# Performance work log

Hardware: AMD Instinct MI355X
Metric: run time of the kernel (lower is better)

## Reference

```python
import jax, jax.numpy as jnp
import numpy as np

D_MODEL = 1024
B, N = 2, 4096
EPS = 1e-4


def setup_inputs() -> dict:
    key = jax.random.key(0)
    ks = jax.random.split(key, 8)
    s = 1.0 / np.sqrt(D_MODEL)
    return {
        "x": jax.random.normal(ks[0], (B, N, D_MODEL), dtype=jnp.float32),
        "Wq": jax.random.normal(ks[1], (D_MODEL, D_MODEL), dtype=jnp.float32) * s,
        "bq": jax.random.normal(ks[2], (D_MODEL,), dtype=jnp.float32) * 0.01,
        "Wk": jax.random.normal(ks[3], (D_MODEL, D_MODEL), dtype=jnp.float32) * s,
        "bk": jax.random.normal(ks[4], (D_MODEL,), dtype=jnp.float32) * 0.01,
        "Wv": jax.random.normal(ks[5], (D_MODEL, D_MODEL), dtype=jnp.float32) * s,
        "bv": jax.random.normal(ks[6], (D_MODEL,), dtype=jnp.float32) * 0.01,
        "alpha": jnp.float32(1.5),
        "lam": jnp.float32(12.0),
    }


def reference(x, Wq, bq, Wk, bk, Wv, bv, alpha, lam):
    # CSOCKernelAttention.forward
    Bb, n, d = x.shape
    # torch nn.Linear: y = x @ W.T + b
    q = jnp.einsum("bnd,ed->bne", x, Wq) + bq
    k = jnp.einsum("bnd,ed->bne", x, Wk) + bk
    v = jnp.einsum("bnd,ed->bne", x, Wv) + bv
    idx = jnp.arange(n, dtype=jnp.float32)
    r = jnp.abs(idx[:, None] - idx[None, :])  # [N, N]
    # K(r) = (r + eps)^(-|alpha|) * exp(-r / |lambda|)
    K = (r + EPS) ** (-jnp.abs(alpha)) * jnp.exp(-r / jnp.abs(lam))  # [N, N]
    logits = jnp.einsum("bqd,bkd->bqk", q, k) / jnp.sqrt(jnp.float32(d))
    logits = logits * K[None]
    attn = jax.nn.softmax(logits, axis=-1)
    out = jnp.einsum("bqk,bkd->bqd", attn, v)
    return (out, attn, K)
```

## Files before the change

### kernel.cpp

```cpp
#include <hip/hip_runtime.h>
#include <hip/hip_bf16.h>
#include <cstdint>
#include <cstddef>

#define D_MODEL 1024
#define SEQ_N   4096
#define BATCH   2
#define BAND    256
#define NELEM   ((size_t)BATCH * SEQ_N * D_MODEL)

typedef __attribute__((ext_vector_type(4))) float  floatx4;
typedef __attribute__((ext_vector_type(8))) short  short8;
typedef __attribute__((ext_vector_type(4))) short  short4v;

__device__ __forceinline__ unsigned short f2bf(float f) {
  unsigned u = __float_as_uint(f);
  u += 0x7FFFu + ((u >> 16) & 1u);
  return (unsigned short)(u >> 16);
}
__device__ __forceinline__ float bf2f(unsigned short u) {
  return __uint_as_float(((unsigned)u) << 16);
}

__global__ __launch_bounds__(256)
void fused_prep(const float* __restrict__ x,
                const float* __restrict__ Wq, const float* __restrict__ Wk,
                const float* __restrict__ Wv, const float* __restrict__ bv,
                const float* __restrict__ alpha_p, const float* __restrict__ lam_p,
                unsigned short* __restrict__ xb,
                unsigned short* __restrict__ Bcat2,
                unsigned short* __restrict__ wqT,
                unsigned short* __restrict__ wkT,
                float* __restrict__ bias2,
                float* __restrict__ K1d)
{
  __shared__ unsigned short Tld[64][66];
  int bid = blockIdx.x, tid = threadIdx.x;
  if (bid < 4096) {
    int i = bid * 256 + tid;
    const floatx4* s4 = (const floatx4*)x;
    floatx4 a = s4[i * 2], b = s4[i * 2 + 1];
    short8 pk;
    pk[0] = (short)f2bf(a[0]); pk[1] = (short)f2bf(a[1]);
    pk[2] = (short)f2bf(a[2]); pk[3] = (short)f2bf(a[3]);
    pk[4] = (short)f2bf(b[0]); pk[5] = (short)f2bf(b[1]);
    pk[6] = (short)f2bf(b[2]); pk[7] = (short)f2bf(b[3]);
    *(short8*)(xb + (size_t)i * 8) = pk;
  } else if (bid < 4608) {
    int i = (bid - 4096) * 256 + tid;
    const floatx4* s4 = (const floatx4*)Wv;
    floatx4 a = s4[i * 2], b = s4[i * 2 + 1];
    short8 pk;
    pk[0] = (short)f2bf(a[0]); pk[1] = (short)f2bf(a[1]);
    pk[2] = (short)f2bf(a[2]); pk[3] = (short)f2bf(a[3]);
    pk[4] = (short)f2bf(b[0]); pk[5] = (short)f2bf(b[1]);
    pk[6] = (short)f2bf(b[2]); pk[7] = (short)f2bf(b[3]);
    *(short8*)(Bcat2 + (size_t)D_MODEL * D_MODEL + (size_t)i * 8) = pk;
  } else if (bid < 5120) {
    int u = bid - 4608;
    const float* src = (u < 256) ? Wq : Wk;
    unsigned short* dst = (u < 256) ? wqT : wkT;
    int t = u & 255;
    int tr = t >> 4, tc = t & 15;
    int rl = tid >> 2, cc = (tid & 3) * 16;
    const float* sp = src + (size_t)(tr * 64 + rl) * D_MODEL + tc * 64 + cc;
#pragma unroll
    for (int q4 = 0; q4 < 4; ++q4) {
      floatx4 v = *(const floatx4*)(sp + q4 * 4);
#pragma unroll
      for (int e = 0; e < 4; ++e) Tld[cc + q4 * 4 + e][rl] = f2bf(v[e]);
    }
    __syncthreads();
    int cl = tid >> 2, rchunk = (tid & 3) * 16;
    short8 o0, o1;
#pragma unroll
    for (int e = 0; e < 8; ++e) { o0[e] = (short)Tld[cl][rchunk + e]; o1[e] = (short)Tld[cl][rchunk + 8 + e]; }
    unsigned short* dp = dst + (size_t)(tc * 64 + cl) * D_MODEL + tr * 64 + rchunk;
    *(short8*)dp = o0;
    *(short8*)(dp + 8) = o1;
  } else {
    int t = (bid - 5120) * 256 + tid;
    if (t < SEQ_N) {
      float a   = fabsf(alpha_p[0]);
      float lam = fabsf(lam_p[0]);
      float rf  = (float)t;
      K1d[t] = powf(rf + 1e-4f, -a) * expf(-rf / lam);
    }
    int v = t - SEQ_N;
    if (v >= 0 && v < D_MODEL) bias2[D_MODEL + v] = bv[v];
  }
}

__global__ __launch_bounds__(256)
void wg_kernel(const unsigned short* __restrict__ wkT,
               const unsigned short* __restrict__ wqT,
               const float* __restrict__ bq, const float* __restrict__ bk,
               unsigned short* __restrict__ Mt,
               float* __restrict__ bias2, float* __restrict__ wqv)
{
  __shared__ unsigned short As[64 * 32];
  __shared__ unsigned short Bs[64 * 32];
  const int bid = blockIdx.x, tid = threadIdx.x;
  const int lane = tid & 63, wave = tid >> 6;

  if (bid < 512) {
    const int idx = bid * 4 + wave;
    const int d = idx & (D_MODEL - 1);
    const bool isK = idx < D_MODEL;
    const unsigned short* row = (isK ? wkT : wqT) + (size_t)d * D_MODEL + lane * 16;
    const float* b = isK ? bq : bk;
    float s = 0.f;
    short8 v0 = *(const short8*)row, v1 = *(const short8*)(row + 8);
#pragma unroll
    for (int e = 0; e < 8; ++e) {
      s += bf2f((unsigned short)v0[e]) * b[lane * 16 + e];
      s += bf2f((unsigned short)v1[e]) * b[lane * 16 + 8 + e];
    }
#pragma unroll
    for (int o = 32; o; o >>= 1) s += __shfl_xor(s, o);
    if (lane == 0) { if (isK) bias2[d] = s; else wqv[d] = s; }
    return;
  }

  int flat = bid - 512;
  int w = (flat & 7) * 32 + (flat >> 3);
  int bx = w % 16, by = w / 16;
  const int bm0 = by * 64, bn0 = bx * 64;
  const int wm = (wave >> 1) * 32, wn = (wave & 1) * 32;

  floatx4 acc[2][2] = {};
  for (int k0 = 0; k0 < D_MODEL; k0 += 32) {
    {
      int bu = wave * 64;
      int u  = bu + lane;
      const unsigned short* srcA = wkT + (size_t)(bm0 + (u >> 2)) * D_MODEL + k0 + (u & 3) * 8;
      __builtin_amdgcn_global_load_lds((const __attribute__((address_space(1))) void*)srcA,
                                       (__attribute__((address_space(3))) void*)(As + bu * 8), 16, 0, 0);
      const unsigned short* srcB = wqT + (size_t)(bn0 + (u >> 2)) * D_MODEL + k0 + (u & 3) * 8;
      __builtin_amdgcn_global_load_lds((const __attribute__((address_space(1))) void*)srcB,
                                       (__attribute__((address_space(3))) void*)(Bs + bu * 8), 16, 0, 0);
    }
    __syncthreads();
    short8 af[2], bf[2];
#pragma unroll
    for (int i = 0; i < 2; ++i)
      af[i] = *(const short8*)(As + (wm + i * 16 + (lane & 15)) * 32 + (lane >> 4) * 8);
#pragma unroll
    for (int j = 0; j < 2; ++j)
      bf[j] = *(const short8*)(Bs + (wn + j * 16 + (lane & 15)) * 32 + (lane >> 4) * 8);
#pragma unroll
    for (int i = 0; i < 2; ++i)
#pragma unroll
      for (int j = 0; j < 2; ++j)
        acc[i][j] = __builtin_amdgcn_mfma_f32_16x16x32_bf16(af[i], bf[j], acc[i][j], 0, 0, 0);
    __syncthreads();
  }
#pragma unroll
  for (int i = 0; i < 2; ++i) {
#pragma unroll
    for (int j = 0; j < 2; ++j) {
      int col   = bn0 + wn + j * 16 + (lane & 15);
      int rbase = bm0 + wm + i * 16 + (lane >> 4) * 4;
#pragma unroll
      for (int r = 0; r < 4; ++r)
        Mt[(size_t)(rbase + r) * D_MODEL + col] = f2bf(acc[i][j][r]);
    }
  }
}

__global__ __launch_bounds__(256)
void rc_kernel(const unsigned short* __restrict__ vT,
               const unsigned short* __restrict__ xb,
               const float* __restrict__ wqv,
               const float* __restrict__ bq, const float* __restrict__ bk,
               float* __restrict__ colsumV, float* __restrict__ rho)
{
  const int bid = blockIdx.x;
  const int lane = threadIdx.x & 63, wave = threadIdx.x >> 6;
  if (bid < 512) {
    const int idx = bid * 4 + wave;
    const int d = idx >> 1, b = idx & 1;
    const unsigned short* p = vT + (size_t)d * (BATCH * SEQ_N) + b * SEQ_N;
    float s = 0.f;
#pragma unroll
    for (int it = 0; it < 8; ++it) {
      short8 v = *(const short8*)(p + (size_t)(it * 512 + lane * 8));
#pragma unroll
      for (int e = 0; e < 8; ++e) s += bf2f((unsigned short)v[e]);
    }
#pragma unroll
    for (int o = 32; o; o >>= 1) s += __shfl_xor(s, o);
    if (lane == 0) colsumV[b * D_MODEL + d] = s;
    return;
  }
  const int gi = (bid - 512) * 4 + wave;
  const unsigned short* xr = xb + (size_t)gi * D_MODEL + lane * 16;
  float s1 = 0.f, s2 = 0.f;
  short8 v0 = *(const short8*)xr, v1 = *(const short8*)(xr + 8);
#pragma unroll
  for (int e = 0; e < 8; ++e) {
    s1 += bf2f((unsigned short)v0[e]) * wqv[lane * 16 + e];
    s1 += bf2f((unsigned short)v1[e]) * wqv[lane * 16 + 8 + e];
  }
#pragma unroll
  for (int e = 0; e < 16; ++e)
    s2 += bq[lane * 16 + e] * bk[lane * 16 + e];
  float s = s1 + s2;
#pragma unroll
  for (int o = 32; o; o >>= 1) s += __shfl_xor(s, o);
  if (lane == 0) rho[gi] = s;
}

__global__ void k1d_kernel(float* __restrict__ K1d,
                           const float* __restrict__ alpha_p,
                           const float* __restrict__ lam_p) {
  int r = blockIdx.x * blockDim.x + threadIdx.x;
  if (r >= SEQ_N) return;
  float a   = fabsf(alpha_p[0]);
  float lam = fabsf(lam_p[0]);
  float rf  = (float)r;
  K1d[r] = powf(rf + 1e-4f, -a) * expf(-rf / lam);
}

__global__ __launch_bounds__(256) void writeK_kernel(float* __restrict__ Kout,
                                                     const float* __restrict__ K1d) {
  size_t t = (size_t)blockIdx.x * 256 + threadIdx.x;
  size_t f = t * 4;
  int i = (int)(f >> 12);
  int j = (int)(f & 4095);
  floatx4 v;
#pragma unroll
  for (int e = 0; e < 4; ++e) {
    int d = i - (j + e); d = d < 0 ? -d : d;
    v[e] = K1d[d];
  }
  __builtin_nontemporal_store(v, (floatx4*)(Kout + f));
}

__global__ __launch_bounds__(256)
void uv_gemm(const unsigned short* __restrict__ xb,
             const unsigned short* __restrict__ Bcat2,
             const float* __restrict__ bias2,
             unsigned short* __restrict__ ub,
             unsigned short* __restrict__ vT)
{
  __shared__ unsigned short As[128 * 64];
  __shared__ unsigned short Bs[128 * 64];
  const int tid = threadIdx.x, lane = tid & 63, wave = tid >> 6;

  int gx = (int)gridDim.x, gy = (int)gridDim.y;
  int total = gx * gy;
  int flat  = (int)blockIdx.y * gx + (int)blockIdx.x;
  int w     = (flat & 7) * (total >> 3) + (flat >> 3);
  int bx = w % gx, by = w / gx;
  const int bm0 = by * 128;
  const int bn0 = bx * 128;
  const int wm = (wave >> 1) * 64, wn = (wave & 1) * 64;
  const bool isU = (bn0 < D_MODEL);

  floatx4 acc[4][4] = {};
  for (int k0 = 0; k0 < D_MODEL; k0 += 64) {
#pragma unroll
    for (int t = 0; t < 4; ++t) {
      int bu  = wave * 64 + t * 256;
      int u   = bu + lane;
      int row = u >> 3;
      int c   = (u & 7) ^ (row & 7);
      const unsigned short* srcA = xb + (size_t)(bm0 + row) * D_MODEL + k0 + c * 8;
      __builtin_amdgcn_global_load_lds((const __attribute__((address_space(1))) void*)srcA,
                                       (__attribute__((address_space(3))) void*)(As + bu * 8), 16, 0, 0);
      const unsigned short* srcB = Bcat2 + (size_t)(bn0 + row) * D_MODEL + k0 + c * 8;
      __builtin_amdgcn_global_load_lds((const __attribute__((address_space(1))) void*)srcB,
                                       (__attribute__((address_space(3))) void*)(Bs + bu * 8), 16, 0, 0);
    }
    __syncthreads();
#pragma unroll
    for (int s = 0; s < 2; ++s) {
      short8 af[4], bf[4];
#pragma unroll
      for (int i = 0; i < 4; ++i) {
        int row = wm + i * 16 + (lane & 15);
        int pc  = (s * 4 + (lane >> 4)) ^ (row & 7);
        af[i] = *(const short8*)(As + row * 64 + pc * 8);
      }
#pragma unroll
      for (int j = 0; j < 4; ++j) {
        int row = wn + j * 16 + (lane & 15);
        int pc  = (s * 4 + (lane >> 4)) ^ (row & 7);
        bf[j] = *(const short8*)(Bs + row * 64 + pc * 8);
      }
      if (isU) {
#pragma unroll
        for (int i = 0; i < 4; ++i)
#pragma unroll
          for (int j = 0; j < 4; ++j)
            acc[i][j] = __builtin_amdgcn_mfma_f32_16x16x32_bf16(bf[j], af[i], acc[i][j], 0, 0, 0);
      } else {
#pragma unroll
        for (int i = 0; i < 4; ++i)
#pragma unroll
          for (int j = 0; j < 4; ++j)
            acc[i][j] = __builtin_amdgcn_mfma_f32_16x16x32_bf16(af[i], bf[j], acc[i][j], 0, 0, 0);
      }
    }
    __syncthreads();
  }

  if (isU) {
#pragma unroll
    for (int i = 0; i < 4; ++i) {
#pragma unroll
      for (int j = 0; j < 4; ++j) {
        int xrow = bm0 + wm + i * 16 + (lane & 15);
        int n0   = bn0 + wn + j * 16 + (lane >> 4) * 4;
        floatx4 b4 = *(const floatx4*)(bias2 + n0);
        short4v pk;
#pragma unroll
        for (int r = 0; r < 4; ++r) pk[r] = (short)f2bf(acc[i][j][r] + b4[r]);
        *(short4v*)(ub + (size_t)xrow * D_MODEL + n0) = pk;
      }
    }
  } else {
#pragma unroll
    for (int i = 0; i < 4; ++i) {
#pragma unroll
      for (int j = 0; j < 4; ++j) {
        int n     = bn0 + wn + j * 16 + (lane & 15);
        int e     = n - D_MODEL;
        int rbase = bm0 + wm + i * 16 + (lane >> 4) * 4;
        float b = bias2[n];
        short4v pk;
#pragma unroll
        for (int r = 0; r < 4; ++r) pk[r] = (short)f2bf(acc[i][j][r] + b);
        *(short4v*)(vT + (size_t)e * (BATCH * SEQ_N) + rbase) = pk;
      }
    }
  }
}

__global__ __launch_bounds__(256)
void band_logits(const unsigned short* __restrict__ U,
                 const unsigned short* __restrict__ Xb,
                 const float* __restrict__ rho,
                 float* __restrict__ Sband,
                 const float* __restrict__ K1d)
{
  __shared__ unsigned short As[64 * 64];
  __shared__ unsigned short Bs[128 * 64];
  const int tid = threadIdx.x, lane = tid & 63, wave = tid >> 6;
  const int bx = blockIdx.x;
  const int g  = blockIdx.y;
  const int z  = blockIdx.z;
  const int bm0 = g * 64;
  const int bn0 = g * 64 - 64 + bx * 128;
  const int wm = (wave >> 1) * 32, wn = (wave & 1) * 64;

  const unsigned short* Ag = U  + (size_t)z * SEQ_N * D_MODEL;
  const unsigned short* Bg = Xb + (size_t)z * SEQ_N * D_MODEL;

  floatx4 acc[2][4] = {};
  for (int k0 = 0; k0 < D_MODEL; k0 += 64) {
#pragma unroll
    for (int t = 0; t < 2; ++t) {
      int bu  = wave * 64 + t * 256;
      int u   = bu + lane;
      int row = u >> 3;
      int c   = (u & 7) ^ (row & 7);
      const unsigned short* srcA = Ag + (size_t)(bm0 + row) * D_MODEL + k0 + c * 8;
      __builtin_amdgcn_global_load_lds((const __attribute__((address_space(1))) void*)srcA,
                                       (__attribute__((address_space(3))) void*)(As + bu * 8), 16, 0, 0);
    }
#pragma unroll
    for (int t = 0; t < 4; ++t) {
      int bu  = wave * 64 + t * 256;
      int u   = bu + lane;
      int row = u >> 3;
      int c   = (u & 7) ^ (row & 7);
      const unsigned short* srcB = Bg + (long)(bn0 + row) * D_MODEL + k0 + c * 8;
      __builtin_amdgcn_global_load_lds((const __attribute__((address_space(1))) void*)srcB,
                                       (__attribute__((address_space(3))) void*)(Bs + bu * 8), 16, 0, 0);
    }
    __syncthreads();
#pragma unroll
    for (int s = 0; s < 2; ++s) {
      short8 af[2], bf[4];
#pragma unroll
      for (int i = 0; i < 2; ++i) {
        int row = wm + i * 16 + (lane & 15);
        int pc  = (s * 4 + (lane >> 4)) ^ (row & 7);
        af[i] = *(const short8*)(As + row * 64 + pc * 8);
      }
#pragma unroll
      for (int j = 0; j < 4; ++j) {
        int row = wn + j * 16 + (lane & 15);
        int pc  = (s * 4 + (lane >> 4)) ^ (row & 7);
        bf[j] = *(const short8*)(Bs + row * 64 + pc * 8);
      }
#pragma unroll
      for (int i = 0; i < 2; ++i)
#pragma unroll
        for (int j = 0; j < 4; ++j)
          acc[i][j] = __builtin_amdgcn_mfma_f32_16x16x32_bf16(af[i], bf[j], acc[i][j], 0, 0, 0);
    }
    __syncthreads();
  }

  float* Cb = Sband + ((size_t)z * SEQ_N + bm0) * BAND + bx * 128;
#pragma unroll
  for (int i = 0; i < 2; ++i) {
    int rl0 = wm + i * 16 + (lane >> 4) * 4;
    float rr[4];
#pragma unroll
    for (int r = 0; r < 4; ++r) rr[r] = rho[(size_t)z * SEQ_N + bm0 + rl0 + r];
#pragma unroll
    for (int j = 0; j < 4; ++j) {
      int cl  = wn + j * 16 + (lane & 15);
#pragma unroll
      for (int r = 0; r < 4; ++r) {
        int col = bn0 + cl;
        int d = (bm0 + rl0 + r) - col; d = d < 0 ? -d : d;
        float v = ((unsigned)col < (unsigned)SEQ_N)
                    ? (acc[i][j][r] + rr[r]) * 0.03125f * K1d[d] : 0.f;
        Cb[(size_t)(rl0 + r) * BAND + cl] = v;
      }
    }
  }
}

__global__ __launch_bounds__(256)
void softmax_band(const float* __restrict__ Sband,
                  float* __restrict__ attn,
                  unsigned short* __restrict__ Pb,
                  float* __restrict__ c_arr)
{
  __shared__ float lds_e[4][BAND];
  const int lane = threadIdx.x & 63, wave = threadIdx.x >> 6;
  const int gi = blockIdx.x * 4 + wave;
  const int ii = gi & (SEQ_N - 1);
  const int g  = ii >> 6;
  const int cbase = g * 64 - 64;
  const float* S = Sband + (size_t)gi * BAND;

  float sv[4];
  float m = 0.0f;
#pragma unroll
  for (int j = 0; j < 4; ++j) {
    int t = j * 64 + lane;
    int col = cbase + t;
    sv[j] = S[t];
    if ((unsigned)col < (unsigned)SEQ_N) m = fmaxf(m, sv[j]);
  }
#pragma unroll
  for (int o = 32; o; o >>= 1) m = fmaxf(m, __shfl_xor(m, o));

  float s = 0.f;
#pragma unroll
  for (int j = 0; j < 4; ++j) {
    int t = j * 64 + lane;
    int col = cbase + t;
    float e = ((unsigned)col < (unsigned)SEQ_N) ? __expf(sv[j] - m) : 0.f;
    sv[j] = e;
    s += e;
  }
#pragma unroll
  for (int o = 32; o; o >>= 1) s += __shfl_xor(s, o);

  int n_valid = BAND - ((g == 0) ? 64 : 0) - ((g == 63) ? 64 : 0);
  float efar  = __expf(-m);
  float denom = s + (float)(SEQ_N - n_valid) * efar;
  float inv   = 1.0f / denom;
  float c     = efar * inv;

  unsigned short* prow = Pb + (size_t)gi * BAND;
#pragma unroll
  for (int j = 0; j < 4; ++j) {
    int t = j * 64 + lane;
    float p = sv[j] * inv;
    lds_e[wave][t] = p;
    int col = cbase + t;
    prow[t] = ((unsigned)col < (unsigned)SEQ_N) ? f2bf(p - c) : (unsigned short)0;
  }
  if (lane == 0) c_arr[gi] = c;

  float* arow = attn + (size_t)gi * SEQ_N;
#pragma unroll
  for (int jj = 0; jj < 16; ++jj) {
    int col0 = jj * 256 + lane * 4;
    floatx4 o;
#pragma unroll
    for (int e = 0; e < 4; ++e) {
      int t = col0 + e - cbase;
      o[e] = ((unsigned)t < (unsigned)BAND) ? lds_e[wave][t] : c;
    }
    __builtin_nontemporal_store(o, (floatx4*)(arow + col0));
  }
}

__global__ __launch_bounds__(256)
void band_pv(const unsigned short* __restrict__ Pb,
             const unsigned short* __restrict__ vT,
             const float* __restrict__ c_arr,
             const float* __restrict__ colsumV,
             float* __restrict__ outp)
{
  __shared__ unsigned short As[64 * 64];
  __shared__ unsigned short Bs[128 * 64];
  const int tid = threadIdx.x, lane = tid & 63, wave = tid >> 6;
  const int bx = blockIdx.x;
  const int g  = blockIdx.y;
  const int z  = blockIdx.z;
  const int bm0 = g * 64;
  const int bn0 = bx * 128;
  const int wm = (wave >> 1) * 32, wn = (wave & 1) * 64;

  const unsigned short* Ag = Pb + ((size_t)z * SEQ_N + bm0) * BAND;
  const unsigned short* Bg = vT + (long)z * SEQ_N + (long)bm0 - 64;

  floatx4 acc[2][4] = {};
  for (int k0 = 0; k0 < BAND; k0 += 64) {
#pragma unroll
    for (int t = 0; t < 2; ++t) {
      int bu  = wave * 64 + t * 256;
      int u   = bu + lane;
      int row = u >> 3;
      int c   = (u & 7) ^ (row & 7);
      const unsigned short* srcA = Ag + (size_t)row * BAND + k0 + c * 8;
      __builtin_amdgcn_global_load_lds((const __attribute__((address_space(1))) void*)srcA,
                                       (__attribute__((address_space(3))) void*)(As + bu * 8), 16, 0, 0);
    }
#pragma unroll
    for (int t = 0; t < 4; ++t) {
      int bu  = wave * 64 + t * 256;
      int u   = bu + lane;
      int row = u >> 3;
      int c   = (u & 7) ^ (row & 7);
      const unsigned short* srcB = Bg + (size_t)(bn0 + row) * (BATCH * SEQ_N) + k0 + c * 8;
      __builtin_amdgcn_global_load_lds((const __attribute__((address_space(1))) void*)srcB,
                                       (__attribute__((address_space(3))) void*)(Bs + bu * 8), 16, 0, 0);
    }
    __syncthreads();
#pragma unroll
    for (int s = 0; s < 2; ++s) {
      short8 af[2], bf[4];
#pragma unroll
      for (int i = 0; i < 2; ++i) {
        int row = wm + i * 16 + (lane & 15);
        int pc  = (s * 4 + (lane >> 4)) ^ (row & 7);
        af[i] = *(const short8*)(As + row * 64 + pc * 8);
      }
#pragma unroll
      for (int j = 0; j < 4; ++j) {
        int row = wn + j * 16 + (lane & 15);
        int pc  = (s * 4 + (lane >> 4)) ^ (row & 7);
        bf[j] = *(const short8*)(Bs + row * 64 + pc * 8);
      }
#pragma unroll
      for (int i = 0; i < 2; ++i)
#pragma unroll
        for (int j = 0; j < 4; ++j)
          acc[i][j] = __builtin_amdgcn_mfma_f32_16x16x32_bf16(af[i], bf[j], acc[i][j], 0, 0, 0);
    }
    __syncthreads();
  }

#pragma unroll
  for (int i = 0; i < 2; ++i) {
#pragma unroll
    for (int j = 0; j < 4; ++j) {
      int col   = bn0 + wn + j * 16 + (lane & 15);
      int rbase = bm0 + wm + i * 16 + (lane >> 4) * 4;
      float csv = colsumV[z * D_MODEL + col];
#pragma unroll
      for (int r = 0; r < 4; ++r) {
        int row = rbase + r;
        float o = acc[i][j][r] + c_arr[(size_t)z * SEQ_N + row] * csv;
        __builtin_nontemporal_store(o, outp + ((size_t)z * SEQ_N + row) * D_MODEL + col);
      }
    }
  }
}

#define BM 128
#define BN 128
#define BK 32

template<int ASRC, int BSRC, int EPI>
__global__ __launch_bounds__(256)
void gemm_bt(const void* __restrict__ Ap_, int lda, long sA,
             const void* __restrict__ Bp_, int ldb, long sB,
             void* __restrict__ Cp_, int ldc, long sC,
             int K, const float* __restrict__ bias,
             const float* __restrict__ K1d)
{
  __shared__ unsigned short As[BM * BK];
  __shared__ unsigned short Bs[BN * BK];
  const int tid  = threadIdx.x;
  const int lane = tid & 63;
  const int wave = tid >> 6;

  int gx = (int)gridDim.x, gy = (int)gridDim.y;
  int total = gx * gy * (int)gridDim.z;
  int flat  = (int)blockIdx.z * gx * gy + (int)blockIdx.y * gx + (int)blockIdx.x;
  int w     = (flat & 7) * (total >> 3) + (flat >> 3);
  int bx = w % gx;
  int t_ = w / gx;
  int by = t_ % gy;
  int z  = t_ / gy;

  const int bm0  = by * BM;
  const int bn0  = bx * BN;
  const int wm   = (wave >> 1) * 64;
  const int wn   = (wave & 1) * 64;

  floatx4 acc[4][4] = {};

  const unsigned short* Agb = (const unsigned short*)Ap_ + (size_t)z * (size_t)sA;
  const float*          Agf = (const float*)Ap_          + (size_t)z * (size_t)sA;
  const unsigned short* Bgb = (const unsigned short*)Bp_ + (size_t)z * (size_t)sB;
  const float*          Bgf = (const float*)Bp_          + (size_t)z * (size_t)sB;

  for (int k0 = 0; k0 < K; k0 += BK) {
    if constexpr (ASRC == 0) {
#pragma unroll
      for (int t = 0; t < 2; ++t) {
        int bu = wave * 64 + t * 256;
        int u  = bu + lane;
        const unsigned short* src = Agb + (size_t)(bm0 + (u >> 2)) * lda + k0 + (u & 3) * 8;
        __builtin_amdgcn_global_load_lds((const __attribute__((address_space(1))) void*)src,
                                         (__attribute__((address_space(3))) void*)(As + bu * 8),
                                         16, 0, 0);
      }
    } else {
#pragma unroll
      for (int t = 0; t < 2; ++t) {
        int u = tid + t * 256;
        const float* src = Agf + (size_t)(bm0 + (u >> 2)) * lda + k0 + (u & 3) * 8;
        floatx4 x0 = *(const floatx4*)src;
        floatx4 x1 = *(const floatx4*)(src + 4);
        short8 pk;
        pk[0] = (short)f2bf(x0[0]); pk[1] = (short)f2bf(x0[1]);
        pk[2] = (short)f2bf(x0[2]); pk[3] = (short)f2bf(x0[3]);
        pk[4] = (short)f2bf(x1[0]); pk[5] = (short)f2bf(x1[1]);
        pk[6] = (short)f2bf(x1[2]); pk[7] = (short)f2bf(x1[3]);
        *(short8*)(As + u * 8) = pk;
      }
    }
    if constexpr (BSRC == 0) {
#pragma unroll
      for (int t = 0; t < 2; ++t) {
        int bu = wave * 64 + t * 256;
        int u  = bu + lane;
        const unsigned short* src = Bgb + (size_t)(bn0 + (u >> 2)) * ldb + k0 + (u & 3) * 8;
        __builtin_amdgcn_global_load_lds((const __attribute__((address_space(1))) void*)src,
                                         (__attribute__((address_space(3))) void*)(Bs + bu * 8),
                                         16, 0, 0);
      }
    } else {
#pragma unroll
      for (int t = 0; t < 2; ++t) {
        int u = tid + t * 256;
        const float* src = Bgf + (size_t)(bn0 + (u >> 2)) * ldb + k0 + (u & 3) * 8;
        floatx4 x0 = *(const floatx4*)src;
        floatx4 x1 = *(const floatx4*)(src + 4);
        short8 pk;
        pk[0] = (short)f2bf(x0[0]); pk[1] = (short)f2bf(x0[1]);
        pk[2] = (short)f2bf(x0[2]); pk[3] = (short)f2bf(x0[3]);
        pk[4] = (short)f2bf(x1[0]); pk[5] = (short)f2bf(x1[1]);
        pk[6] = (short)f2bf(x1[2]); pk[7] = (short)f2bf(x1[3]);
        *(short8*)(Bs + u * 8) = pk;
      }
    }
    __syncthreads();

    short8 af[4], bf[4];
#pragma unroll
    for (int i = 0; i < 4; ++i)
      af[i] = *(const short8*)(As + (wm + i * 16 + (lane & 15)) * BK + (lane >> 4) * 8);
#pragma unroll
    for (int j = 0; j < 4; ++j)
      bf[j] = *(const short8*)(Bs + (wn + j * 16 + (lane & 15)) * BK + (lane >> 4) * 8);
#pragma unroll
    for (int i = 0; i < 4; ++i)
#pragma unroll
      for (int j = 0; j < 4; ++j)
        acc[i][j] = __builtin_amdgcn_mfma_f32_16x16x32_bf16(af[i], bf[j], acc[i][j], 0, 0, 0);
    __syncthreads();
  }

  const int col0 = bn0 + wn;
  const int row0 = bm0 + wm;
#pragma unroll
  for (int i = 0; i < 4; ++i) {
#pragma unroll
    for (int j = 0; j < 4; ++j) {
      int col   = col0 + j * 16 + (lane & 15);
      int rbase = row0 + i * 16 + (lane >> 4) * 4;
      if constexpr (EPI == 0) {
        unsigned short* C = (unsigned short*)Cp_ + (size_t)z * (size_t)sC;
        float b = bias[col];
#pragma unroll
        for (int r = 0; r < 4; ++r)
          C[(size_t)(rbase + r) * ldc + col] = f2bf(acc[i][j][r] + b);
      } else if constexpr (EPI == 1) {
        unsigned short* C = (unsigned short*)Cp_ + (size_t)z * (size_t)sC;
#pragma unroll
        for (int r = 0; r < 4; ++r)
          C[(size_t)(rbase + r) * ldc + col] = f2bf(acc[i][j][r] + bias[rbase + r]);
      } else if constexpr (EPI == 2) {
        float* C = (float*)Cp_ + (size_t)z * (size_t)sC;
#pragma unroll
        for (int r = 0; r < 4; ++r) {
          int row = rbase + r;
          int d = row - col; d = d < 0 ? -d : d;
          C[(size_t)row * ldc + col] = acc[i][j][r] * 0.03125f * K1d[d];
        }
      } else {
        float* C = (float*)Cp_ + (size_t)z * (size_t)sC;
#pragma unroll
        for (int r = 0; r < 4; ++r)
          C[(size_t)(rbase + r) * ldc + col] = acc[i][j][r];
      }
    }
  }
}

__global__ __launch_bounds__(256)
void softmax_kernel(float* __restrict__ attn) {
  const int tid = threadIdx.x;
  float* p = attn + (size_t)blockIdx.x * SEQ_N;
  floatx4* p4 = (floatx4*)p;
  floatx4 x[4];
  float m = -3.402823466e+38f;
#pragma unroll
  for (int c = 0; c < 4; ++c) {
    x[c] = p4[tid + c * 256];
    m = fmaxf(m, fmaxf(fmaxf(x[c][0], x[c][1]), fmaxf(x[c][2], x[c][3])));
  }
#pragma unroll
  for (int o = 32; o; o >>= 1) m = fmaxf(m, __shfl_xor(m, o));
  __shared__ float redm[4], reds[4];
  if ((tid & 63) == 0) redm[tid >> 6] = m;
  __syncthreads();
  m = fmaxf(fmaxf(redm[0], redm[1]), fmaxf(redm[2], redm[3]));
  float s = 0.f;
#pragma unroll
  for (int c = 0; c < 4; ++c)
#pragma unroll
    for (int e = 0; e < 4; ++e) {
      float t = __expf(x[c][e] - m);
      x[c][e] = t;
      s += t;
    }
#pragma unroll
  for (int o = 32; o; o >>= 1) s += __shfl_xor(s, o);
  if ((tid & 63) == 0) reds[tid >> 6] = s;
  __syncthreads();
  s = reds[0] + reds[1] + reds[2] + reds[3];
  float inv = 1.0f / s;
#pragma unroll
  for (int c = 0; c < 4; ++c) {
    floatx4 y;
#pragma unroll
    for (int e = 0; e < 4; ++e) y[e] = x[c][e] * inv;
    p4[tid + c * 256] = y;
  }
}

extern "C" void kernel_launch(void* const* d_in, const int* in_sizes, int n_in,
                              void* d_out, int out_size, void* d_ws, size_t ws_size,
                              hipStream_t stream) {
  const float* x     = (const float*)d_in[0];
  const float* Wq    = (const float*)d_in[1];
  const float* bq    = (const float*)d_in[2];
  const float* Wk    = (const float*)d_in[3];
  const float* bk    = (const float*)d_in[4];
  const float* Wv    = (const float*)d_in[5];
  const float* bv    = (const float*)d_in[6];
  const float* alpha = (const float*)d_in[7];
  const float* lam   = (const float*)d_in[8];

  float* outp  = (float*)d_out;
  float* attnp = outp + (size_t)BATCH * SEQ_N * D_MODEL;
  float* Kp    = attnp + (size_t)BATCH * SEQ_N * SEQ_N;

  char* ws = (char*)d_ws;
  float* K1d = (float*)ws;
  unsigned short* vT   = (unsigned short*)(ws + 16384);
  unsigned short* xb   = vT + NELEM;
  unsigned short* ub   = xb + NELEM;
  unsigned short* wqT  = ub + NELEM;
  unsigned short* wkT  = wqT + (size_t)D_MODEL * D_MODEL;
  unsigned short* Bcat2 = wkT + (size_t)D_MODEL * D_MODEL;
  float* Sband   = (float*)(Bcat2 + (size_t)2 * D_MODEL * D_MODEL);
  unsigned short* Pb = (unsigned short*)(Sband + (size_t)BATCH * SEQ_N * BAND);
  float* c_arr   = (float*)(Pb + (size_t)BATCH * SEQ_N * BAND);
  float* colsumV = c_arr + (size_t)BATCH * SEQ_N;
  float* bias2   = colsumV + (size_t)BATCH * D_MODEL;
  float* wqv     = bias2 + 2 * D_MODEL;
  float* rho     = wqv + D_MODEL;

  size_t need = (size_t)((char*)(rho + BATCH * SEQ_N) - ws);
  const bool fast = ws_size >= need;

  if (fast) {
    fused_prep<<<5140, 256, 0, stream>>>(x, Wq, Wk, Wv, bv, alpha, lam,
                                         xb, Bcat2, wqT, wkT, bias2, K1d);
    writeK_kernel<<<(SEQ_N * SEQ_N / 4) / 256, 256, 0, stream>>>(Kp, K1d);
    wg_kernel<<<768, 256, 0, stream>>>(wkT, wqT, bq, bk, Bcat2, bias2, wqv);
    uv_gemm<<<dim3(16, 64), 256, 0, stream>>>(xb, Bcat2, bias2, ub, vT);
    rc_kernel<<<2560, 256, 0, stream>>>(vT, xb, wqv, bq, bk, colsumV, rho);
    band_logits<<<dim3(2, SEQ_N / 64, BATCH), 256, 0, stream>>>(ub, xb, rho, Sband, K1d);
    softmax_band<<<BATCH * SEQ_N / 4, 256, 0, stream>>>(Sband, attnp, Pb, c_arr);
    band_pv<<<dim3(D_MODEL / 128, SEQ_N / 64, BATCH), 256, 0, stream>>>(
        Pb, vT, c_arr, colsumV, outp);
  } else {
    unsigned short* qb = xb;
    unsigned short* kb = ub;
    k1d_kernel<<<16, 256, 0, stream>>>(K1d, alpha, lam);
    writeK_kernel<<<(SEQ_N * SEQ_N / 4) / 256, 256, 0, stream>>>(Kp, K1d);
    gemm_bt<1, 1, 0><<<dim3(D_MODEL / BN, BATCH * SEQ_N / BM, 1), 256, 0, stream>>>(
        x, D_MODEL, 0, Wq, D_MODEL, 0, qb, D_MODEL, 0, D_MODEL, bq, nullptr);
    gemm_bt<1, 1, 0><<<dim3(D_MODEL / BN, BATCH * SEQ_N / BM, 1), 256, 0, stream>>>(
        x, D_MODEL, 0, Wk, D_MODEL, 0, kb, D_MODEL, 0, D_MODEL, bk, nullptr);
    gemm_bt<1, 1, 1><<<dim3(BATCH * SEQ_N / BN, D_MODEL / BM, 1), 256, 0, stream>>>(
        Wv, D_MODEL, 0, x, D_MODEL, 0, vT, BATCH * SEQ_N, 0, D_MODEL, bv, nullptr);
    gemm_bt<0, 0, 2><<<dim3(SEQ_N / BN, SEQ_N / BM, BATCH), 256, 0, stream>>>(
        qb, D_MODEL, (long)SEQ_N * D_MODEL, kb, D_MODEL, (long)SEQ_N * D_MODEL,
        attnp, SEQ_N, (long)SEQ_N * SEQ_N, D_MODEL, nullptr, K1d);
    softmax_kernel<<<BATCH * SEQ_N, 256, 0, stream>>>(attnp);
    gemm_bt<1, 0, 3><<<dim3(D_MODEL / BN, SEQ_N / BM, BATCH), 256, 0, stream>>>(
        attnp, SEQ_N, (long)SEQ_N * SEQ_N, vT, BATCH * SEQ_N, (long)SEQ_N,
        outp, D_MODEL, (long)SEQ_N * D_MODEL, SEQ_N, nullptr, nullptr);
  }
}
```

Before: 163.5 us.

## Merge independent small kernels into heterogeneous launches by block-index ranges

```diff
diff --git a/kernel.cpp b/kernel.cpp
--- a/kernel.cpp
+++ b/kernel.cpp
@@ -169,90 +169,43 @@
 }
 
 __global__ __launch_bounds__(256)
-void rc_kernel(const unsigned short* __restrict__ vT,
-               const unsigned short* __restrict__ xb,
-               const float* __restrict__ wqv,
-               const float* __restrict__ bq, const float* __restrict__ bk,
-               float* __restrict__ colsumV, float* __restrict__ rho)
-{
-  const int bid = blockIdx.x;
-  const int lane = threadIdx.x & 63, wave = threadIdx.x >> 6;
-  if (bid < 512) {
-    const int idx = bid * 4 + wave;
-    const int d = idx >> 1, b = idx & 1;
-    const unsigned short* p = vT + (size_t)d * (BATCH * SEQ_N) + b * SEQ_N;
-    float s = 0.f;
-#pragma unroll
-    for (int it = 0; it < 8; ++it) {
-      short8 v = *(const short8*)(p + (size_t)(it * 512 + lane * 8));
-#pragma unroll
-      for (int e = 0; e < 8; ++e) s += bf2f((unsigned short)v[e]);
-    }
-#pragma unroll
-    for (int o = 32; o; o >>= 1) s += __shfl_xor(s, o);
-    if (lane == 0) colsumV[b * D_MODEL + d] = s;
-    return;
-  }
-  const int gi = (bid - 512) * 4 + wave;
-  const unsigned short* xr = xb + (size_t)gi * D_MODEL + lane * 16;
-  float s1 = 0.f, s2 = 0.f;
-  short8 v0 = *(const short8*)xr, v1 = *(const short8*)(xr + 8);
-#pragma unroll
-  for (int e = 0; e < 8; ++e) {
-    s1 += bf2f((unsigned short)v0[e]) * wqv[lane * 16 + e];
-    s1 += bf2f((unsigned short)v1[e]) * wqv[lane * 16 + 8 + e];
-  }
-#pragma unroll
-  for (int e = 0; e < 16; ++e)
-    s2 += bq[lane * 16 + e] * bk[lane * 16 + e];
-  float s = s1 + s2;
-#pragma unroll
-  for (int o = 32; o; o >>= 1) s += __shfl_xor(s, o);
-  if (lane == 0) rho[gi] = s;
-}
-
-__global__ void k1d_kernel(float* __restrict__ K1d,
-                           const float* __restrict__ alpha_p,
-                           const float* __restrict__ lam_p) {
-  int r = blockIdx.x * blockDim.x + threadIdx.x;
-  if (r >= SEQ_N) return;
-  float a   = fabsf(alpha_p[0]);
-  float lam = fabsf(lam_p[0]);
-  float rf  = (float)r;
-  K1d[r] = powf(rf + 1e-4f, -a) * expf(-rf / lam);
-}
-
-__global__ __launch_bounds__(256) void writeK_kernel(float* __restrict__ Kout,
-                                                     const float* __restrict__ K1d) {
-  size_t t = (size_t)blockIdx.x * 256 + threadIdx.x;
-  size_t f = t * 4;
-  int i = (int)(f >> 12);
-  int j = (int)(f & 4095);
-  floatx4 v;
-#pragma unroll
-  for (int e = 0; e < 4; ++e) {
-    int d = i - (j + e); d = d < 0 ? -d : d;
-    v[e] = K1d[d];
-  }
-  __builtin_nontemporal_store(v, (floatx4*)(Kout + f));
-}
-
-__global__ __launch_bounds__(256)
-void uv_gemm(const unsigned short* __restrict__ xb,
-             const unsigned short* __restrict__ Bcat2,
-             const float* __restrict__ bias2,
-             unsigned short* __restrict__ ub,
-             unsigned short* __restrict__ vT)
+void uvr_kernel(const unsigned short* __restrict__ xb,
+                const unsigned short* __restrict__ Bcat2,
+                const float* __restrict__ bias2,
+                unsigned short* __restrict__ ub,
+                unsigned short* __restrict__ vT,
+                const float* __restrict__ wqv,
+                const float* __restrict__ bq, const float* __restrict__ bk,
+                float* __restrict__ rho)
 {
   __shared__ unsigned short As[128 * 64];
   __shared__ unsigned short Bs[128 * 64];
-  const int tid = threadIdx.x, lane = tid & 63, wave = tid >> 6;
-
-  int gx = (int)gridDim.x, gy = (int)gridDim.y;
-  int total = gx * gy;
-  int flat  = (int)blockIdx.y * gx + (int)blockIdx.x;
-  int w     = (flat & 7) * (total >> 3) + (flat >> 3);
-  int bx = w % gx, by = w / gx;
+  const int bid = blockIdx.x, tid = threadIdx.x;
+  const int lane = tid & 63, wave = tid >> 6;
+
+  if (bid >= 1024) {
+    const int gi = (bid - 1024) * 4 + wave;
+    const unsigned short* xr = xb + (size_t)gi * D_MODEL + lane * 16;
+    float s1 = 0.f, s2 = 0.f;
+    short8 v0 = *(const short8*)xr, v1 = *(const short8*)(xr + 8);
+#pragma unroll
+    for (int e = 0; e < 8; ++e) {
+      s1 += bf2f((unsigned short)v0[e]) * wqv[lane * 16 + e];
+      s1 += bf2f((unsigned short)v1[e]) * wqv[lane * 16 + 8 + e];
+    }
+#pragma unroll
+    for (int e = 0; e < 16; ++e)
+      s2 += bq[lane * 16 + e] * bk[lane * 16 + e];
+    float s = s1 + s2;
+#pragma unroll
+    for (int o = 32; o; o >>= 1) s += __shfl_xor(s, o);
+    if (lane == 0) rho[gi] = s;
+    return;
+  }
+
+  int flat  = bid;
+  int w     = (flat & 7) * 128 + (flat >> 3);
+  int bx = w % 16, by = w / 16;
   const int bm0 = by * 128;
   const int bn0 = bx * 128;
   const int wm = (wave >> 1) * 64, wn = (wave & 1) * 64;
@@ -339,18 +292,40 @@
 }
 
 __global__ __launch_bounds__(256)
-void band_logits(const unsigned short* __restrict__ U,
-                 const unsigned short* __restrict__ Xb,
-                 const float* __restrict__ rho,
-                 float* __restrict__ Sband,
-                 const float* __restrict__ K1d)
+void lc_kernel(const unsigned short* __restrict__ vT,
+               float* __restrict__ colsumV,
+               const unsigned short* __restrict__ U,
+               const unsigned short* __restrict__ Xb,
+               const float* __restrict__ rho,
+               float* __restrict__ Sband,
+               const float* __restrict__ K1d)
 {
   __shared__ unsigned short As[64 * 64];
   __shared__ unsigned short Bs[128 * 64];
-  const int tid = threadIdx.x, lane = tid & 63, wave = tid >> 6;
-  const int bx = blockIdx.x;
-  const int g  = blockIdx.y;
-  const int z  = blockIdx.z;
+  const int bid = blockIdx.x, tid = threadIdx.x;
+  const int lane = tid & 63, wave = tid >> 6;
+
+  if (bid < 512) {
+    const int idx = bid * 4 + wave;
+    const int d = idx >> 1, b = idx & 1;
+    const unsigned short* p = vT + (size_t)d * (BATCH * SEQ_N) + b * SEQ_N;
+    float s = 0.f;
+#pragma unroll
+    for (int it = 0; it < 8; ++it) {
+      short8 v = *(const short8*)(p + (size_t)(it * 512 + lane * 8));
+#pragma unroll
+      for (int e = 0; e < 8; ++e) s += bf2f((unsigned short)v[e]);
+    }
+#pragma unroll
+    for (int o = 32; o; o >>= 1) s += __shfl_xor(s, o);
+    if (lane == 0) colsumV[b * D_MODEL + d] = s;
+    return;
+  }
+
+  const int u_  = bid - 512;
+  const int bx  = u_ & 1;
+  const int g   = (u_ >> 1) & 63;
+  const int z   = u_ >> 7;
   const int bm0 = g * 64;
   const int bn0 = g * 64 - 64 + bx * 128;
   const int wm = (wave >> 1) * 32, wn = (wave & 1) * 64;
@@ -428,14 +403,33 @@
 }
 
 __global__ __launch_bounds__(256)
-void softmax_band(const float* __restrict__ Sband,
-                  float* __restrict__ attn,
-                  unsigned short* __restrict__ Pb,
-                  float* __restrict__ c_arr)
+void sk_kernel(const float* __restrict__ Sband,
+               float* __restrict__ attn,
+               unsigned short* __restrict__ Pb,
+               float* __restrict__ c_arr,
+               float* __restrict__ Kout,
+               const float* __restrict__ K1d)
 {
   __shared__ float lds_e[4][BAND];
-  const int lane = threadIdx.x & 63, wave = threadIdx.x >> 6;
-  const int gi = blockIdx.x * 4 + wave;
+  const int bid = blockIdx.x, tid = threadIdx.x;
+  const int lane = tid & 63, wave = tid >> 6;
+
+  if (bid >= 2048) {
+    size_t t = (size_t)(bid - 2048) * 256 + tid;
+    size_t f = t * 4;
+    int i = (int)(f >> 12);
+    int j = (int)(f & 4095);
+    floatx4 v;
+#pragma unroll
+    for (int e = 0; e < 4; ++e) {
+      int d = i - (j + e); d = d < 0 ? -d : d;
+      v[e] = K1d[d];
+    }
+    __builtin_nontemporal_store(v, (floatx4*)(Kout + f));
+    return;
+  }
+
+  const int gi = bid * 4 + wave;
   const int ii = gi & (SEQ_N - 1);
   const int g  = ii >> 6;
   const int cbase = g * 64 - 64;
@@ -580,6 +574,32 @@
   }
 }
 
+__global__ void k1d_kernel(float* __restrict__ K1d,
+                           const float* __restrict__ alpha_p,
+                           const float* __restrict__ lam_p) {
+  int r = blockIdx.x * blockDim.x + threadIdx.x;
+  if (r >= SEQ_N) return;
+  float a   = fabsf(alpha_p[0]);
+  float lam = fabsf(lam_p[0]);
+  float rf  = (float)r;
+  K1d[r] = powf(rf + 1e-4f, -a) * expf(-rf / lam);
+}
+
+__global__ __launch_bounds__(256) void writeK_kernel(float* __restrict__ Kout,
+                                                     const float* __restrict__ K1d) {
+  size_t t = (size_t)blockIdx.x * 256 + threadIdx.x;
+  size_t f = t * 4;
+  int i = (int)(f >> 12);
+  int j = (int)(f & 4095);
+  floatx4 v;
+#pragma unroll
+  for (int e = 0; e < 4; ++e) {
+    int d = i - (j + e); d = d < 0 ? -d : d;
+    v[e] = K1d[d];
+  }
+  __builtin_nontemporal_store(v, (floatx4*)(Kout + f));
+}
+
 #define BM 128
 #define BN 128
 #define BK 32
@@ -805,12 +825,10 @@
   if (fast) {
     fused_prep<<<5140, 256, 0, stream>>>(x, Wq, Wk, Wv, bv, alpha, lam,
                                          xb, Bcat2, wqT, wkT, bias2, K1d);
-    writeK_kernel<<<(SEQ_N * SEQ_N / 4) / 256, 256, 0, stream>>>(Kp, K1d);
     wg_kernel<<<768, 256, 0, stream>>>(wkT, wqT, bq, bk, Bcat2, bias2, wqv);
-    uv_gemm<<<dim3(16, 64), 256, 0, stream>>>(xb, Bcat2, bias2, ub, vT);
-    rc_kernel<<<2560, 256, 0, stream>>>(vT, xb, wqv, bq, bk, colsumV, rho);
-    band_logits<<<dim3(2, SEQ_N / 64, BATCH), 256, 0, stream>>>(ub, xb, rho, Sband, K1d);
-    softmax_band<<<BATCH * SEQ_N / 4, 256, 0, stream>>>(Sband, attnp, Pb, c_arr);
+    uvr_kernel<<<3072, 256, 0, stream>>>(xb, Bcat2, bias2, ub, vT, wqv, bq, bk, rho);
+    lc_kernel<<<768, 256, 0, stream>>>(vT, colsumV, ub, xb, rho, Sband, K1d);
+    sk_kernel<<<18432, 256, 0, stream>>>(Sband, attnp, Pb, c_arr, Kp, K1d);
     band_pv<<<dim3(D_MODEL / 128, SEQ_N / 64, BATCH), 256, 0, stream>>>(
         Pb, vT, c_arr, colsumV, outp);
   } else {
```

Result: faster. 158.8 us (-2.9%).
